# Optimization experiments

Hardware: AMD Instinct MI355X
Metric: run time of the kernel (lower is better)

Reference implementation:

```python
import jax, jax.numpy as jnp
import numpy as np

BIG = 1e30  # finite stand-in for +inf to keep grads clean


def _chamfer_loss(bin_center, ground_truth):
    # bin_center: [B, n_bins, 1] 1-D 'point cloud' of bin centers
    # ground_truth: [B, 1, H, W] depth map
    B = bin_center.shape[0]
    c = bin_center[..., 0]                      # [B, nb]
    p = ground_truth.reshape(B, -1)             # [B, V] flattened depth points
    mask = p >= 0.001                           # valid (non-near-zero) depths
    n = jnp.sum(mask, axis=1)                   # [B] valid count per sample
    Lmax = jnp.max(n)                           # pad_sequence pads every sample to L_max
    npad = (Lmax - n).astype(c.dtype)           # number of zero pad-points per sample

    # pairwise squared distances between bin centers and depth points
    D = (c[:, :, None] - p[:, None, :]) ** 2    # [B, nb, V]

    # direction 1: gt points -> nearest bin center (sum over points)
    dmin_p = jnp.min(D, axis=1)                 # [B, V]
    sumA = jnp.sum(jnp.where(mask, dmin_p, 0.0), axis=1)
    # each zero pad-point contributes min_j c_j^2
    c2 = c ** 2                                 # [B, nb]
    sumA = sumA + npad * jnp.min(c2, axis=1)

    # direction 2: bin centers -> nearest gt point (incl. zero pad-points if any)
    Dm = jnp.where(mask[:, None, :], D, jnp.asarray(BIG, D.dtype))
    min_valid = jnp.min(Dm, axis=2)             # [B, nb] min over valid points
    has_pad = (npad > 0)[:, None]
    min_b = jnp.where(has_pad, jnp.minimum(min_valid, c2), min_valid)
    sumB = jnp.sum(min_b, axis=1)               # [B]

    # chamferdist: point_reduction=sum, batch_reduction=mean, bidirectional
    return jnp.mean(sumA + sumB)


def setup_inputs() -> dict:
    key = jax.random.key(0)
    k1, k2 = jax.random.split(key)
    bin_center = jax.random.uniform(k1, (4, 256, 1), dtype=jnp.float32)
    ground_truth = jax.random.uniform(k2, (4, 1, 352, 448), dtype=jnp.float32)
    return {"bin_center": bin_center, "ground_truth": ground_truth}


def reference(bin_center, ground_truth):
    return _chamfer_loss(bin_center, ground_truth)
```

## Files before the change

### kernel.cpp

```cpp
#include <hip/hip_runtime.h>

#define NB   256
#define TPB  256
#define NI   (NB + 1)
#define G    128
#define P    5
#define MINF 1e30f
#define CAPD 1e15f

__global__ __launch_bounds__(TPB) void k_main(
    const float* __restrict__ bc, const float* __restrict__ gt,
    int V, int CH,
    float* __restrict__ sumA_part, int* __restrict__ cnt_part,
    unsigned* __restrict__ gmin, unsigned* __restrict__ gmaxN,
    float* __restrict__ sbins)
{
    const int b   = blockIdx.x / G;
    const int blk = blockIdx.x % G;
    const int tid = threadIdx.x;

    __shared__ float    raw[NB], c[NB];
    __shared__ unsigned imn[NI], imx[NI];

    const float v = bc[b * NB + tid];
    raw[tid] = v;
    for (int t = tid; t < NI; t += TPB) { imn[t] = 0xFFFFFFFFu; imx[t] = 0u; }
    __syncthreads();
    int rank = 0;
    #pragma unroll 16
    for (int j = 0; j < NB; ++j) {
        const float rj = raw[j];
        rank += (rj < v || (rj == v && j < tid)) ? 1 : 0;
    }
    c[rank] = v;
    __syncthreads();
    if (blk == 0) sbins[b * NB + tid] = c[tid];

    const int start = blk * CH;
    const int cn = min(CH, V - start);
    const float* __restrict__ gp = gt + (size_t)b * V + start;

    float q[P];
    #pragma unroll
    for (int p = 0; p < P; ++p) {
        const int i = tid + p * TPB;
        q[p] = (i < cn) ? gp[i] : -1.f;
    }

    int idx[P];
    #pragma unroll
    for (int p = 0; p < P; ++p) idx[p] = 0;
    #pragma unroll
    for (int st = 128; st >= 1; st >>= 1) {
        #pragma unroll
        for (int p = 0; p < P; ++p)
            idx[p] += (c[idx[p] + st - 1] <= q[p]) ? st : 0;
    }
    #pragma unroll
    for (int p = 0; p < P; ++p)
        idx[p] += (c[idx[p]] <= q[p]) ? 1 : 0;

    float sum = 0.f; int cnt = 0;
    #pragma unroll
    for (int p = 0; p < P; ++p) {
        if (q[p] >= 0.001f) {
            const float dlo = (idx[p] > 0)  ? (q[p] - c[idx[p] - 1]) : MINF;
            const float dhi = (idx[p] < NB) ? (c[idx[p]] - q[p])     : MINF;
            const float d = fminf(dlo, dhi);
            sum += d * d; ++cnt;
            atomicMin(&imn[idx[p]], __float_as_uint(q[p]));
            atomicMax(&imx[idx[p]], __float_as_uint(q[p]));
        }
    }
    __syncthreads();

    for (int t = tid; t < NI; t += TPB) {
        const unsigned lo = imn[t], hi = imx[t];
        if (lo != 0xFFFFFFFFu) atomicMin(&gmin [b * NI + t], lo);
        if (hi != 0u)          atomicMin(&gmaxN[b * NI + t], ~hi);
    }

    for (int off = 32; off; off >>= 1) {
        sum += __shfl_down(sum, off);
        cnt += __shfl_down(cnt, off);
    }
    __shared__ float r4[4]; __shared__ int i4[4];
    if ((tid & 63) == 0) { r4[tid >> 6] = sum; i4[tid >> 6] = cnt; }
    __syncthreads();
    if (tid == 0) {
        sumA_part[blockIdx.x] = r4[0] + r4[1] + r4[2] + r4[3];
        cnt_part [blockIdx.x] = i4[0] + i4[1] + i4[2] + i4[3];
    }
}

__global__ __launch_bounds__(TPB) void k_final(
    const float* __restrict__ sbins,
    const float* __restrict__ sumA_part, const int* __restrict__ cnt_part,
    const unsigned* __restrict__ gmin, const unsigned* __restrict__ gmaxN,
    int B, float* __restrict__ out)
{
    const int tid  = threadIdx.x;
    const int lane = tid & 63, w = tid >> 6;
    __shared__ float r4[4]; __shared__ int i4[4]; __shared__ float q4[4];
    __shared__ float ssa[8]; __shared__ int sn[8];
    __shared__ float wtop[4], wbot[4];

    for (int bb = 0; bb < B; ++bb) {
        float s = 0.f; int cc = 0;
        for (int k = tid; k < G; k += TPB) {
            s  += sumA_part[bb * G + k];
            cc += cnt_part [bb * G + k];
        }
        for (int off = 32; off; off >>= 1) { s += __shfl_down(s, off); cc += __shfl_down(cc, off); }
        if (lane == 0) { r4[w] = s; i4[w] = cc; }
        __syncthreads();
        if (tid == 0) { ssa[bb] = r4[0]+r4[1]+r4[2]+r4[3]; sn[bb] = i4[0]+i4[1]+i4[2]+i4[3]; }
        __syncthreads();
    }
    int Lmax = 0;
    for (int bb = 0; bb < B; ++bb) Lmax = max(Lmax, sn[bb]);

    float total = 0.f;
    for (int bb = 0; bb < B; ++bb) {
        const unsigned gx  = gmaxN[bb * NI + tid];
        const unsigned lob = gmin [bb * NI + tid + 1];
        float pv = (gx  == 0xFFFFFFFFu) ? -MINF : __uint_as_float(~gx);
        float sv = (lob == 0xFFFFFFFFu) ?  MINF : __uint_as_float(lob);

        #pragma unroll
        for (int off = 1; off < 64; off <<= 1) {
            const float o = __shfl_up(pv, off);
            if (lane >= off) pv = fmaxf(pv, o);
        }
        #pragma unroll
        for (int off = 1; off < 64; off <<= 1) {
            const float o = __shfl_down(sv, off);
            if (lane < 64 - off) sv = fminf(sv, o);
        }
        if (lane == 63) wtop[w] = pv;
        if (lane == 0)  wbot[w] = sv;
        __syncthreads();
        #pragma unroll
        for (int ww = 0; ww < 4; ++ww) {
            if (ww < w) pv = fmaxf(pv, wtop[ww]);
            if (ww > w) sv = fminf(sv, wbot[ww]);
        }

        const float cj = sbins[bb * NB + tid];
        const float c2 = cj * cj;
        const float d  = fminf(fminf(cj - pv, sv - cj), CAPD);
        float bm = d * d;
        const int npad = Lmax - sn[bb];
        if (npad > 0) bm = fminf(bm, c2);
        float s = bm, mc = c2;
        for (int off = 32; off; off >>= 1) {
            s  += __shfl_down(s, off);
            mc  = fminf(mc, __shfl_down(mc, off));
        }
        if (lane == 0) { r4[w] = s; q4[w] = mc; }
        __syncthreads();
        if (tid == 0)
            total += ssa[bb]
                   + (float)npad * fminf(fminf(q4[0], q4[1]), fminf(q4[2], q4[3]))
                   + (r4[0] + r4[1] + r4[2] + r4[3]);
        __syncthreads();
    }
    if (tid == 0) out[0] = total / (float)B;
}

extern "C" void kernel_launch(void* const* d_in, const int* in_sizes, int n_in,
                              void* d_out, int out_size, void* d_ws, size_t ws_size,
                              hipStream_t stream) {
    const float* bc = (const float*)d_in[0];
    const float* gt = (const float*)d_in[1];
    const int B  = in_sizes[0] / NB;
    const int V  = in_sizes[1] / B;
    const int CH = (V + G - 1) / G;

    float*    sbins     = (float*)d_ws;
    float*    sumA_part = sbins + (size_t)B * NB;
    int*      cnt_part  = (int*)(sumA_part + (size_t)B * G);
    unsigned* gmin      = (unsigned*)(cnt_part + (size_t)B * G);
    unsigned* gmaxN     = gmin + (size_t)B * NI;

    hipMemsetAsync(gmin, 0xFF, (size_t)B * NI * 2 * sizeof(unsigned), stream);

    k_main <<<B * G, TPB, 0, stream>>>(bc, gt, V, CH,
                                       sumA_part, cnt_part, gmin, gmaxN, sbins);
    k_final<<<1, TPB, 0, stream>>>(sbins, sumA_part, cnt_part,
                                   gmin, gmaxN, B, (float*)d_out);
}
```

Before: 79.59 us.

## Sort bins once in separate kernel, replace memset, preload final inputs to LDS

Moves the per-block O(NB^2) rank sort of bin centers out of the 512 main blocks into a small per-batch sort kernel. That kernel also initializes the global min/max arrays, replacing the hipMemsetAsync. The max now uses atomicMax directly instead of inverting the value and taking a min. The final kernel stages all partial sums and bin min/max data into shared memory up front instead of reading global memory inside each batch loop. The main kernel's sort work is removed, at the cost of an extra kernel launch and a dependency on the sort finishing first.

Result: no change. 79.16 us (-0.5%).

```diff
diff --git a/kernel.cpp b/kernel.cpp
--- a/kernel.cpp
+++ b/kernel.cpp
@@ -8,23 +8,18 @@
 #define MINF 1e30f
 #define CAPD 1e15f
 
-__global__ __launch_bounds__(TPB) void k_main(
-    const float* __restrict__ bc, const float* __restrict__ gt,
-    int V, int CH,
-    float* __restrict__ sumA_part, int* __restrict__ cnt_part,
-    unsigned* __restrict__ gmin, unsigned* __restrict__ gmaxN,
-    float* __restrict__ sbins)
-{
-    const int b   = blockIdx.x / G;
-    const int blk = blockIdx.x % G;
-    const int tid = threadIdx.x;
-
-    __shared__ float    raw[NB], c[NB];
-    __shared__ unsigned imn[NI], imx[NI];
-
+__global__ __launch_bounds__(NB) void k_sort(const float* __restrict__ bc,
+                                             float* __restrict__ sbins,
+                                             unsigned* __restrict__ gmin,
+                                             unsigned* __restrict__ gmax) {
+    __shared__ float raw[NB];
+    const int tid = threadIdx.x, b = blockIdx.x;
     const float v = bc[b * NB + tid];
     raw[tid] = v;
-    for (int t = tid; t < NI; t += TPB) { imn[t] = 0xFFFFFFFFu; imx[t] = 0u; }
+    for (int t = tid; t < NI; t += NB) {
+        gmin[b * NI + t] = 0xFFFFFFFFu;
+        gmax[b * NI + t] = 0u;
+    }
     __syncthreads();
     int rank = 0;
     #pragma unroll 16
@@ -32,13 +27,27 @@
         const float rj = raw[j];
         rank += (rj < v || (rj == v && j < tid)) ? 1 : 0;
     }
-    c[rank] = v;
-    __syncthreads();
-    if (blk == 0) sbins[b * NB + tid] = c[tid];
-
+    sbins[b * NB + rank] = v;
+}
+
+__global__ __launch_bounds__(TPB) void k_main(
+    const float* __restrict__ sbins, const float* __restrict__ gt,
+    int V, int CH,
+    float* __restrict__ sumA_part, int* __restrict__ cnt_part,
+    unsigned* __restrict__ gmin, unsigned* __restrict__ gmax)
+{
+    const int b   = blockIdx.x / G;
+    const int blk = blockIdx.x % G;
+    const int tid = threadIdx.x;
     const int start = blk * CH;
     const int cn = min(CH, V - start);
     const float* __restrict__ gp = gt + (size_t)b * V + start;
+
+    __shared__ float    c[NB];
+    __shared__ unsigned imn[NI], imx[NI];
+    c[tid] = sbins[b * NB + tid];
+    for (int t = tid; t < NI; t += TPB) { imn[t] = 0xFFFFFFFFu; imx[t] = 0u; }
+    __syncthreads();
 
     float q[P];
     #pragma unroll
@@ -76,8 +85,8 @@
 
     for (int t = tid; t < NI; t += TPB) {
         const unsigned lo = imn[t], hi = imx[t];
-        if (lo != 0xFFFFFFFFu) atomicMin(&gmin [b * NI + t], lo);
-        if (hi != 0u)          atomicMin(&gmaxN[b * NI + t], ~hi);
+        if (lo != 0xFFFFFFFFu) atomicMin(&gmin[b * NI + t], lo);
+        if (hi != 0u)          atomicMax(&gmax[b * NI + t], hi);
     }
 
     for (int off = 32; off; off >>= 1) {
@@ -96,21 +105,35 @@
 __global__ __launch_bounds__(TPB) void k_final(
     const float* __restrict__ sbins,
     const float* __restrict__ sumA_part, const int* __restrict__ cnt_part,
-    const unsigned* __restrict__ gmin, const unsigned* __restrict__ gmaxN,
+    const unsigned* __restrict__ gmin, const unsigned* __restrict__ gmax,
     int B, float* __restrict__ out)
 {
     const int tid  = threadIdx.x;
     const int lane = tid & 63, w = tid >> 6;
+
+    __shared__ float spart[512]; __shared__ int cpart[512];
+    __shared__ float pmv[4 * NB], smv[4 * NB], sb[4 * NB];
     __shared__ float r4[4]; __shared__ int i4[4]; __shared__ float q4[4];
     __shared__ float ssa[8]; __shared__ int sn[8];
     __shared__ float wtop[4], wbot[4];
 
+    for (int t = tid; t < B * G; t += TPB) {
+        spart[t] = sumA_part[t];
+        cpart[t] = cnt_part [t];
+    }
+    for (int t = tid; t < B * NB; t += TPB) {
+        const int bb = t >> 8, j = t & (NB - 1);
+        sb[t] = sbins[t];
+        const unsigned hib = gmax[bb * NI + j];
+        const unsigned lob = gmin[bb * NI + j + 1];
+        pmv[t] = (hib == 0u)          ? -MINF : __uint_as_float(hib);
+        smv[t] = (lob == 0xFFFFFFFFu) ?  MINF : __uint_as_float(lob);
+    }
+    __syncthreads();
+
     for (int bb = 0; bb < B; ++bb) {
-        float s = 0.f; int cc = 0;
-        for (int k = tid; k < G; k += TPB) {
-            s  += sumA_part[bb * G + k];
-            cc += cnt_part [bb * G + k];
-        }
+        float s = (tid < G) ? spart[bb * G + tid] : 0.f;
+        int   cc = (tid < G) ? cpart[bb * G + tid] : 0;
         for (int off = 32; off; off >>= 1) { s += __shfl_down(s, off); cc += __shfl_down(cc, off); }
         if (lane == 0) { r4[w] = s; i4[w] = cc; }
         __syncthreads();
@@ -122,10 +145,8 @@
 
     float total = 0.f;
     for (int bb = 0; bb < B; ++bb) {
-        const unsigned gx  = gmaxN[bb * NI + tid];
-        const unsigned lob = gmin [bb * NI + tid + 1];
-        float pv = (gx  == 0xFFFFFFFFu) ? -MINF : __uint_as_float(~gx);
-        float sv = (lob == 0xFFFFFFFFu) ?  MINF : __uint_as_float(lob);
+        float pv = pmv[bb * NB + tid];
+        float sv = smv[bb * NB + tid];
 
         #pragma unroll
         for (int off = 1; off < 64; off <<= 1) {
@@ -146,7 +167,7 @@
             if (ww > w) sv = fminf(sv, wbot[ww]);
         }
 
-        const float cj = sbins[bb * NB + tid];
+        const float cj = sb[bb * NB + tid];
         const float c2 = cj * cj;
         const float d  = fminf(fminf(cj - pv, sv - cj), CAPD);
         float bm = d * d;
@@ -181,12 +202,11 @@
     float*    sumA_part = sbins + (size_t)B * NB;
     int*      cnt_part  = (int*)(sumA_part + (size_t)B * G);
     unsigned* gmin      = (unsigned*)(cnt_part + (size_t)B * G);
-    unsigned* gmaxN     = gmin + (size_t)B * NI;
-
-    hipMemsetAsync(gmin, 0xFF, (size_t)B * NI * 2 * sizeof(unsigned), stream);
-
-    k_main <<<B * G, TPB, 0, stream>>>(bc, gt, V, CH,
-                                       sumA_part, cnt_part, gmin, gmaxN, sbins);
+    unsigned* gmax      = gmin + (size_t)B * NI;
+
+    k_sort <<<B, NB, 0, stream>>>(bc, sbins, gmin, gmax);
+    k_main <<<B * G, TPB, 0, stream>>>(sbins, gt, V, CH,
+                                       sumA_part, cnt_part, gmin, gmax);
     k_final<<<1, TPB, 0, stream>>>(sbins, sumA_part, cnt_part,
-                                   gmin, gmaxN, B, (float*)d_out);
-}
+                                   gmin, gmax, B, (float*)d_out);
+}
```

## Fuse final reduction into main kernel via last-block atomic counter

Applied to the files above, without the earlier changes.

Merges the separate finalization kernel into the main kernel. Each block increments a global counter after a threadfence, and the last block to arrive performs the cross-block reduction and writes the result. The counter is initialized by the existing memset, which is extended by one word. This removes a kernel launch and the dependency gap between launches. In exchange it adds shared memory per block and a serialized tail done by one block.

Result: slower. 109.1 us (+37.1%).

```diff
diff --git a/kernel.cpp b/kernel.cpp
--- a/kernel.cpp
+++ b/kernel.cpp
@@ -8,19 +8,22 @@
 #define MINF 1e30f
 #define CAPD 1e15f
 
-__global__ __launch_bounds__(TPB) void k_main(
+__global__ __launch_bounds__(TPB) void k_one(
     const float* __restrict__ bc, const float* __restrict__ gt,
-    int V, int CH,
+    int V, int CH, int B,
     float* __restrict__ sumA_part, int* __restrict__ cnt_part,
     unsigned* __restrict__ gmin, unsigned* __restrict__ gmaxN,
-    float* __restrict__ sbins)
+    float* __restrict__ sbins, unsigned* __restrict__ counter,
+    float* __restrict__ out)
 {
-    const int b   = blockIdx.x / G;
-    const int blk = blockIdx.x % G;
-    const int tid = threadIdx.x;
+    const int tid  = threadIdx.x;
+    const int b    = blockIdx.x / G;
+    const int blk  = blockIdx.x % G;
+    const int lane = tid & 63, w = tid >> 6;
 
     __shared__ float    raw[NB], c[NB];
     __shared__ unsigned imn[NI], imx[NI];
+    __shared__ float r4[4]; __shared__ int i4[4];
 
     const float v = bc[b * NB + tid];
     raw[tid] = v;
@@ -84,33 +87,45 @@
         sum += __shfl_down(sum, off);
         cnt += __shfl_down(cnt, off);
     }
-    __shared__ float r4[4]; __shared__ int i4[4];
-    if ((tid & 63) == 0) { r4[tid >> 6] = sum; i4[tid >> 6] = cnt; }
+    if (lane == 0) { r4[w] = sum; i4[w] = cnt; }
     __syncthreads();
     if (tid == 0) {
         sumA_part[blockIdx.x] = r4[0] + r4[1] + r4[2] + r4[3];
         cnt_part [blockIdx.x] = i4[0] + i4[1] + i4[2] + i4[3];
     }
-}
-
-__global__ __launch_bounds__(TPB) void k_final(
-    const float* __restrict__ sbins,
-    const float* __restrict__ sumA_part, const int* __restrict__ cnt_part,
-    const unsigned* __restrict__ gmin, const unsigned* __restrict__ gmaxN,
-    int B, float* __restrict__ out)
-{
-    const int tid  = threadIdx.x;
-    const int lane = tid & 63, w = tid >> 6;
-    __shared__ float r4[4]; __shared__ int i4[4]; __shared__ float q4[4];
+
+    __threadfence();
+    __syncthreads();
+    __shared__ int lastFlag;
+    if (tid == 0)
+        lastFlag = (atomicAdd(counter, 1u) == (unsigned)gridDim.x - 2u);
+    __syncthreads();
+    if (!lastFlag) return;
+    __threadfence();
+
+    __shared__ float spart[512]; __shared__ int cpart[512];
+    __shared__ float pmv[4 * NB], smv[4 * NB], sb[4 * NB];
+    __shared__ float q4[4];
     __shared__ float ssa[8]; __shared__ int sn[8];
     __shared__ float wtop[4], wbot[4];
 
+    for (int t = tid; t < B * G; t += TPB) {
+        spart[t] = sumA_part[t];
+        cpart[t] = cnt_part [t];
+    }
+    for (int t = tid; t < B * NB; t += TPB) {
+        const int bb = t >> 8, j = t & (NB - 1);
+        sb[t] = sbins[t];
+        const unsigned gx  = gmaxN[bb * NI + j];
+        const unsigned lob = gmin [bb * NI + j + 1];
+        pmv[t] = (gx  == 0xFFFFFFFFu) ? -MINF : __uint_as_float(~gx);
+        smv[t] = (lob == 0xFFFFFFFFu) ?  MINF : __uint_as_float(lob);
+    }
+    __syncthreads();
+
     for (int bb = 0; bb < B; ++bb) {
-        float s = 0.f; int cc = 0;
-        for (int k = tid; k < G; k += TPB) {
-            s  += sumA_part[bb * G + k];
-            cc += cnt_part [bb * G + k];
-        }
+        float s  = (tid < G) ? spart[bb * G + tid] : 0.f;
+        int   cc = (tid < G) ? cpart[bb * G + tid] : 0;
         for (int off = 32; off; off >>= 1) { s += __shfl_down(s, off); cc += __shfl_down(cc, off); }
         if (lane == 0) { r4[w] = s; i4[w] = cc; }
         __syncthreads();
@@ -122,10 +137,8 @@
 
     float total = 0.f;
     for (int bb = 0; bb < B; ++bb) {
-        const unsigned gx  = gmaxN[bb * NI + tid];
-        const unsigned lob = gmin [bb * NI + tid + 1];
-        float pv = (gx  == 0xFFFFFFFFu) ? -MINF : __uint_as_float(~gx);
-        float sv = (lob == 0xFFFFFFFFu) ?  MINF : __uint_as_float(lob);
+        float pv = pmv[bb * NB + tid];
+        float sv = smv[bb * NB + tid];
 
         #pragma unroll
         for (int off = 1; off < 64; off <<= 1) {
@@ -146,7 +159,7 @@
             if (ww > w) sv = fminf(sv, wbot[ww]);
         }
 
-        const float cj = sbins[bb * NB + tid];
+        const float cj = sb[bb * NB + tid];
         const float c2 = cj * cj;
         const float d  = fminf(fminf(cj - pv, sv - cj), CAPD);
         float bm = d * d;
@@ -182,11 +195,11 @@
     int*      cnt_part  = (int*)(sumA_part + (size_t)B * G);
     unsigned* gmin      = (unsigned*)(cnt_part + (size_t)B * G);
     unsigned* gmaxN     = gmin + (size_t)B * NI;
-
-    hipMemsetAsync(gmin, 0xFF, (size_t)B * NI * 2 * sizeof(unsigned), stream);
-
-    k_main <<<B * G, TPB, 0, stream>>>(bc, gt, V, CH,
-                                       sumA_part, cnt_part, gmin, gmaxN, sbins);
-    k_final<<<1, TPB, 0, stream>>>(sbins, sumA_part, cnt_part,
-                                   gmin, gmaxN, B, (float*)d_out);
+    unsigned* counter   = gmaxN + (size_t)B * NI;
+
+    hipMemsetAsync(gmin, 0xFF, ((size_t)B * NI * 2 + 1) * sizeof(unsigned), stream);
+
+    k_one<<<B * G, TPB, 0, stream>>>(bc, gt, V, CH, B,
+                                     sumA_part, cnt_part, gmin, gmaxN,
+                                     sbins, counter, (float*)d_out);
 }
```
